# Performance work log

Hardware: AMD Instinct MI355X
Metric: run time of the kernel (lower is better)

The kernel has to match this reference:

```python
import jax, jax.numpy as jnp
import numpy as np

OUT, IN = 8192, 8192
TOKENS = 32


def setup_inputs() -> dict:
    key = jax.random.key(0)
    k_in, k_w, k_zp, k_s, k_b = jax.random.split(key, 5)
    return {
        "input": jax.random.normal(k_in, (TOKENS, IN), dtype=jnp.float32),
        # int8 quantized weight stored as the compressed parameter
        "weight_packed": jax.random.randint(k_w, (OUT, IN), -128, 128, dtype=jnp.int32).astype(jnp.int8),
        # per-output-channel asymmetric zero point and scale
        "weight_zero_point": jax.random.randint(k_zp, (OUT, 1), -8, 8, dtype=jnp.int32).astype(jnp.int8),
        "weight_scale": (jax.random.uniform(k_s, (OUT, 1), dtype=jnp.float32) * 0.01 + 1e-4),
        "bias": jax.random.normal(k_b, (OUT,), dtype=jnp.float32),
    }


def reference(input, weight_packed, weight_zero_point, weight_scale, bias):
    # Compressor.decompress_module: dequantize int8 weight per output channel
    # w[o, i] = (q[o, i] - zp[o]) * scale[o]   -> fp32 [OUT, IN]
    w = (weight_packed.astype(jnp.int32) - weight_zero_point.astype(jnp.int32)).astype(jnp.float32) * weight_scale
    # F.linear(input, w, bias): [T, IN] @ [OUT, IN]^T + [OUT]
    return jnp.einsum("ti,oi->to", input, w) + bias
```

## Files before the change

### kernel.cpp

```cpp
#include <hip/hip_runtime.h>
#include <stdint.h>

#define TOKENS 32
#define IN_DIM 8192
#define OUT_DIM 8192
#define SLABS 4
#define KSLAB (IN_DIM / SLABS)
#define NWAVE 2
#define KRANGE (KSLAB / NWAVE)
#define BK 128
#define NCHUNK (KRANGE / BK)
#define NTILE (OUT_DIM / 32)

typedef __bf16 bf16x8 __attribute__((ext_vector_type(8)));
typedef float f32x16 __attribute__((ext_vector_type(16)));

static __device__ __forceinline__ uint32_t pk_bf16_2(float f0, float f1) {
    return __builtin_amdgcn_perm(__float_as_uint(f1), __float_as_uint(f0), 0x07060302u);
}
static __device__ __forceinline__ float trunc_bf(float f) {
    return __uint_as_float(__float_as_uint(f) & 0xffff0000u);
}

__global__ __launch_bounds__(256) void prep_kernel(const float* __restrict__ in,
                                                   uint16_t* __restrict__ abf,
                                                   float* __restrict__ rowsum) {
    const int t = blockIdx.x;
    const int tid = threadIdx.x;
    const float4* __restrict__ row = reinterpret_cast<const float4*>(in + (size_t)t * IN_DIM);
    ushort4* __restrict__ orow = reinterpret_cast<ushort4*>(abf + (size_t)t * IN_DIM);
    float s = 0.f;
#pragma unroll
    for (int it = 0; it < IN_DIM / 4 / 256; ++it) {
        const int i4 = it * 256 + tid;
        float4 v = row[i4];
        s += trunc_bf(v.x) + trunc_bf(v.y) + trunc_bf(v.z) + trunc_bf(v.w);
        ushort4 b;
        b.x = (uint16_t)(__float_as_uint(v.x) >> 16);
        b.y = (uint16_t)(__float_as_uint(v.y) >> 16);
        b.z = (uint16_t)(__float_as_uint(v.z) >> 16);
        b.w = (uint16_t)(__float_as_uint(v.w) >> 16);
        orow[i4] = b;
    }
#pragma unroll
    for (int off = 32; off > 0; off >>= 1) s += __shfl_down(s, off);
    __shared__ float wred[4];
    if ((tid & 63) == 0) wred[tid >> 6] = s;
    __syncthreads();
    if (tid == 0) rowsum[t] = wred[0] + wred[1] + wred[2] + wred[3];
}

__global__ __launch_bounds__(128, 1) void gemm_kernel(
        const uint16_t* __restrict__ abf,
        const int* __restrict__ w,
        float* __restrict__ parts) {
    __shared__ int lds[NWAVE][2][32][BK];

    const int tid   = threadIdx.x;
    const int wv    = tid >> 6;
    const int lane  = tid & 63;
    const int lo    = lane & 31;
    const int hi    = lane >> 5;
    const int slab  = blockIdx.x & (SLABS - 1);
    const int tile  = blockIdx.x >> 2;
    const int obase = tile * 32;
    const int k0    = slab * KSLAB + wv * KRANGE;

    auto stage = [&](int c, int b) {
#pragma unroll
        for (int p = 0; p < 16; ++p) {
            const int r   = p * 2 + hi;
            const int swr = (r & 7) << 2;
            const int* g = w + (size_t)(obase + r) * IN_DIM + k0 + c * BK
                             + (((lane & 31) * 4) ^ swr);
            __builtin_amdgcn_global_load_lds(
                (const __attribute__((address_space(1))) void*)g,
                (__attribute__((address_space(3))) void*)&lds[wv][b][p * 2][0],
                16, 0, 0);
        }
    };

    const uint16_t* ain = abf + (size_t)lo * IN_DIM + k0 + hi * 8;
    auto aload = [&](int c, uint4 (&ab)[8]) {
#pragma unroll
        for (int s = 0; s < 8; ++s)
            ab[s] = *reinterpret_cast<const uint4*>(ain + c * BK + s * 16);
    };

    f32x16 acc;
#pragma unroll
    for (int i = 0; i < 16; ++i) acc[i] = 0.f;

    const int sw = (lo & 7) << 2;
    const int* lrow0 = &lds[wv][0][lo][0];
    const int* lrow1 = &lds[wv][1][lo][0];

    auto compute = [&](const int* lrow, const uint4 (&ab)[8]) {
#pragma unroll
        for (int s = 0; s < 8; ++s) {
            const int d0 = s * 16 + hi * 8;
            int4 b0 = *reinterpret_cast<const int4*>(lrow + (d0 ^ sw));
            int4 b1 = *reinterpret_cast<const int4*>(lrow + ((d0 + 4) ^ sw));
            union { uint4 u; bf16x8 v; } af;
            af.u = ab[s];
            union { uint32_t u[4]; bf16x8 v; } bf_;
            bf_.u[0] = pk_bf16_2((float)b0.x, (float)b0.y);
            bf_.u[1] = pk_bf16_2((float)b0.z, (float)b0.w);
            bf_.u[2] = pk_bf16_2((float)b1.x, (float)b1.y);
            bf_.u[3] = pk_bf16_2((float)b1.z, (float)b1.w);
            acc = __builtin_amdgcn_mfma_f32_32x32x16_bf16(af.v, bf_.v, acc, 0, 0, 0);
        }
    };

    uint4 ab0[8], ab1[8];

    stage(0, 0);
    aload(0, ab0);
    for (int cc = 0; cc < NCHUNK; cc += 2) {
        stage(cc + 1, 1);
        aload(cc + 1, ab1);
        asm volatile("s_waitcnt vmcnt(24)" ::: "memory");
        compute(lrow0, ab0);

        if (cc + 2 < NCHUNK) {
            stage(cc + 2, 0);
            aload(cc + 2, ab0);
            asm volatile("s_waitcnt vmcnt(24)" ::: "memory");
        } else {
            asm volatile("s_waitcnt vmcnt(0)" ::: "memory");
        }
        compute(lrow1, ab1);
    }

    __syncthreads();
    float* red = (float*)&lds[0][0][0][0];
#pragma unroll
    for (int r = 0; r < 16; ++r) {
        const int m = (r & 3) + 8 * (r >> 2) + 4 * hi;
        red[wv * (TOKENS * 32) + m * 32 + lo] = acc[r];
    }
    __syncthreads();

    float* pt = parts + (size_t)(slab * NTILE + tile) * (TOKENS * 32);
    for (int idx = tid; idx < TOKENS * 32; idx += 128)
        pt[idx] = red[idx] + red[TOKENS * 32 + idx];
}

__global__ __launch_bounds__(256) void reduce_kernel(
        const float* __restrict__ parts,
        const float* __restrict__ rowsum,
        const int* __restrict__ zp,
        const float* __restrict__ scale,
        const float* __restrict__ bias,
        float* __restrict__ out) {
    const int tile = blockIdx.x;
    const int idx  = threadIdx.x * 4;
    const int m    = idx >> 5;
    const int n    = idx & 31;
    const int o    = tile * 32 + n;

    float4 s = make_float4(0.f, 0.f, 0.f, 0.f);
#pragma unroll
    for (int sl = 0; sl < SLABS; ++sl) {
        float4 p = *reinterpret_cast<const float4*>(
            parts + (size_t)(sl * NTILE + tile) * (TOKENS * 32) + idx);
        s.x += p.x; s.y += p.y; s.z += p.z; s.w += p.w;
    }
    const float rs = rowsum[m];
    const float4 sc = *reinterpret_cast<const float4*>(scale + o);
    const float4 bi = *reinterpret_cast<const float4*>(bias + o);
    const int4   zv = *reinterpret_cast<const int4*>(zp + o);
    float4 r;
    r.x = sc.x * (s.x - (float)zv.x * rs) + bi.x;
    r.y = sc.y * (s.y - (float)zv.y * rs) + bi.y;
    r.z = sc.z * (s.z - (float)zv.z * rs) + bi.z;
    r.w = sc.w * (s.w - (float)zv.w * rs) + bi.w;
    *reinterpret_cast<float4*>(out + (size_t)m * OUT_DIM + o) = r;
}

extern "C" void kernel_launch(void* const* d_in, const int* in_sizes, int n_in,
                              void* d_out, int out_size, void* d_ws, size_t ws_size,
                              hipStream_t stream) {
    const float* in    = (const float*)d_in[0];
    const int*   wq    = (const int*)d_in[1];
    const int*   zp    = (const int*)d_in[2];
    const float* scale = (const float*)d_in[3];
    const float* bias  = (const float*)d_in[4];
    float* out = (float*)d_out;

    uint16_t* abf    = (uint16_t*)d_ws;
    float*    rowsum = (float*)((char*)d_ws + (512u << 10));
    float*    parts  = (float*)((char*)d_ws + (1u << 20));

    prep_kernel<<<TOKENS, 256, 0, stream>>>(in, abf, rowsum);
    gemm_kernel<<<SLABS * NTILE, 128, 0, stream>>>(abf, wq, parts);
    reduce_kernel<<<NTILE, 256, 0, stream>>>(parts, rowsum, zp, scale, bias, out);
}
```

Before: 366.3 us.

## Use single-wave GEMM blocks with larger K chunks and staggered chunk order

The GEMM block drops from two waves splitting K to one wave covering the whole K slab. Chunk size doubles to 256 so each stage issues 32 row loads, and the waitcnt depth rises to match. A hash-based per-block phase XORs the chunk index so blocks start at different K offsets, which is meant to spread DRAM/channel traffic. Removing the second wave also removes the in-block LDS reduction and barriers, at the cost of fewer waves per CU to hide latency and higher register pressure from 16-entry A buffers.

```diff
diff --git a/kernel.cpp b/kernel.cpp
--- a/kernel.cpp
+++ b/kernel.cpp
@@ -6,10 +6,8 @@
 #define OUT_DIM 8192
 #define SLABS 4
 #define KSLAB (IN_DIM / SLABS)
-#define NWAVE 2
-#define KRANGE (KSLAB / NWAVE)
-#define BK 128
-#define NCHUNK (KRANGE / BK)
+#define BK 256
+#define NCHUNK (KSLAB / BK)
 #define NTILE (OUT_DIM / 32)
 
 typedef __bf16 bf16x8 __attribute__((ext_vector_type(8)));
@@ -50,40 +48,39 @@
     if (tid == 0) rowsum[t] = wred[0] + wred[1] + wred[2] + wred[3];
 }
 
-__global__ __launch_bounds__(128, 1) void gemm_kernel(
+__global__ __launch_bounds__(64, 1) void gemm_kernel(
         const uint16_t* __restrict__ abf,
         const int* __restrict__ w,
         float* __restrict__ parts) {
-    __shared__ int lds[NWAVE][2][32][BK];
+    __shared__ int lds[2][32][BK];
 
-    const int tid   = threadIdx.x;
-    const int wv    = tid >> 6;
-    const int lane  = tid & 63;
+    const int lane  = threadIdx.x;
     const int lo    = lane & 31;
     const int hi    = lane >> 5;
     const int slab  = blockIdx.x & (SLABS - 1);
     const int tile  = blockIdx.x >> 2;
     const int obase = tile * 32;
-    const int k0    = slab * KSLAB + wv * KRANGE;
+    const int k0    = slab * KSLAB;
+
+    const uint32_t phase = (blockIdx.x * 2654435761u) >> 29;
 
     auto stage = [&](int c, int b) {
 #pragma unroll
-        for (int p = 0; p < 16; ++p) {
-            const int r   = p * 2 + hi;
-            const int swr = (r & 7) << 2;
-            const int* g = w + (size_t)(obase + r) * IN_DIM + k0 + c * BK
-                             + (((lane & 31) * 4) ^ swr);
+        for (int p = 0; p < 32; ++p) {
+            const int swr = (p & 7) << 2;
+            const int* g = w + (size_t)(obase + p) * IN_DIM + k0 + c * BK
+                             + ((lane * 4) ^ swr);
             __builtin_amdgcn_global_load_lds(
                 (const __attribute__((address_space(1))) void*)g,
-                (__attribute__((address_space(3))) void*)&lds[wv][b][p * 2][0],
+                (__attribute__((address_space(3))) void*)&lds[b][p][0],
                 16, 0, 0);
         }
     };
 
     const uint16_t* ain = abf + (size_t)lo * IN_DIM + k0 + hi * 8;
-    auto aload = [&](int c, uint4 (&ab)[8]) {
+    auto aload = [&](int c, uint4 (&ab)[16]) {
 #pragma unroll
-        for (int s = 0; s < 8; ++s)
+        for (int s = 0; s < 16; ++s)
             ab[s] = *reinterpret_cast<const uint4*>(ain + c * BK + s * 16);
     };
 
@@ -92,12 +89,12 @@
     for (int i = 0; i < 16; ++i) acc[i] = 0.f;
 
     const int sw = (lo & 7) << 2;
-    const int* lrow0 = &lds[wv][0][lo][0];
-    const int* lrow1 = &lds[wv][1][lo][0];
+    const int* lrow0 = &lds[0][lo][0];
+    const int* lrow1 = &lds[1][lo][0];
 
-    auto compute = [&](const int* lrow, const uint4 (&ab)[8]) {
+    auto compute = [&](const int* lrow, const uint4 (&ab)[16]) {
 #pragma unroll
-        for (int s = 0; s < 8; ++s) {
+        for (int s = 0; s < 16; ++s) {
             const int d0 = s * 16 + hi * 8;
             int4 b0 = *reinterpret_cast<const int4*>(lrow + (d0 ^ sw));
             int4 b1 = *reinterpret_cast<const int4*>(lrow + ((d0 + 4) ^ sw));
@@ -112,38 +109,32 @@
         }
     };
 
-    uint4 ab0[8], ab1[8];
+    uint4 ab0[16], ab1[16];
 
-    stage(0, 0);
-    aload(0, ab0);
-    for (int cc = 0; cc < NCHUNK; cc += 2) {
-        stage(cc + 1, 1);
-        aload(cc + 1, ab1);
-        asm volatile("s_waitcnt vmcnt(24)" ::: "memory");
+    stage(phase ^ 0, 0);
+    aload(phase ^ 0, ab0);
+    for (int ci = 0; ci < NCHUNK; ci += 2) {
+        stage(phase ^ (ci + 1), 1);
+        aload(phase ^ (ci + 1), ab1);
+        asm volatile("s_waitcnt vmcnt(48)" ::: "memory");
         compute(lrow0, ab0);
 
-        if (cc + 2 < NCHUNK) {
-            stage(cc + 2, 0);
-            aload(cc + 2, ab0);
-            asm volatile("s_waitcnt vmcnt(24)" ::: "memory");
+        if (ci + 2 < NCHUNK) {
+            stage(phase ^ (ci + 2), 0);
+            aload(phase ^ (ci + 2), ab0);
+            asm volatile("s_waitcnt vmcnt(48)" ::: "memory");
         } else {
             asm volatile("s_waitcnt vmcnt(0)" ::: "memory");
         }
         compute(lrow1, ab1);
     }
 
-    __syncthreads();
-    float* red = (float*)&lds[0][0][0][0];
+    float* pt = parts + (size_t)(slab * NTILE + tile) * (TOKENS * 32);
 #pragma unroll
     for (int r = 0; r < 16; ++r) {
         const int m = (r & 3) + 8 * (r >> 2) + 4 * hi;
-        red[wv * (TOKENS * 32) + m * 32 + lo] = acc[r];
+        pt[m * 32 + lo] = acc[r];
     }
-    __syncthreads();
-
-    float* pt = parts + (size_t)(slab * NTILE + tile) * (TOKENS * 32);
-    for (int idx = tid; idx < TOKENS * 32; idx += 128)
-        pt[idx] = red[idx] + red[TOKENS * 32 + idx];
 }
 
 __global__ __launch_bounds__(256) void reduce_kernel(
@@ -193,6 +184,6 @@
     float*    parts  = (float*)((char*)d_ws + (1u << 20));
 
     prep_kernel<<<TOKENS, 256, 0, stream>>>(in, abf, rowsum);
-    gemm_kernel<<<SLABS * NTILE, 128, 0, stream>>>(abf, wq, parts);
+    gemm_kernel<<<NTILE * SLABS, 64, 0, stream>>>(abf, wq, parts);
     reduce_kernel<<<NTILE, 256, 0, stream>>>(parts, rowsum, zp, scale, bias, out);
 }
```

Measured after the change: 364.8 us. About the same (-0.4%).
